# Optimization experiments

Measured on AMD Instinct MI355X. Metric: run time of the kernel, lower is better.

Reference implementation:

```python
import jax, jax.numpy as jnp
import numpy as np

D_MODEL = 1024
NHEAD = 16
HEAD_DIM = D_MODEL // NHEAD
D_FF = 4096
EPS = 1e-8


def rmsnorm(x, w):
    # matches torch: norm = ||x||_2 / sqrt(d); out = w * x / (rms + eps)
    rms = jnp.linalg.norm(x, axis=-1, keepdims=True) / np.sqrt(x.shape[-1])
    return w * (x / (rms + EPS))


def setup_inputs() -> dict:
    key = jax.random.key(0)
    ks = jax.random.split(key, 11)
    B, S = 4, 2048
    init = lambda k, shape, fan_in: jax.random.uniform(k, shape, jnp.float32, -1.0, 1.0) / np.sqrt(fan_in)
    return {
        "src": jax.random.normal(ks[0], (B, S, D_MODEL), jnp.float32),
        "qkv_w": init(ks[1], (D_MODEL, 3 * D_MODEL), D_MODEL),
        "qkv_b": init(ks[2], (3 * D_MODEL,), D_MODEL),
        "out_w": init(ks[3], (D_MODEL, D_MODEL), D_MODEL),
        "out_b": init(ks[4], (D_MODEL,), D_MODEL),
        "ff1_w": init(ks[5], (D_MODEL, D_FF), D_MODEL),
        "ff1_b": init(ks[6], (D_FF,), D_MODEL),
        "ff2_w": init(ks[7], (D_FF, D_MODEL), D_FF),
        "ff2_b": init(ks[8], (D_MODEL,), D_FF),
        "norm1_w": jnp.ones((D_MODEL,), jnp.float32),
        "norm2_w": jnp.ones((D_MODEL,), jnp.float32),
    }


def reference(src, qkv_w, qkv_b, out_w, out_b, ff1_w, ff1_b, ff2_w, ff2_b, norm1_w, norm2_w):
    B, S, _ = src.shape
    # --- pre-norm attention block ---
    x = rmsnorm(src, norm1_w)
    qkv = x @ qkv_w + qkv_b                     # [B,S,3*D]
    qkv = qkv.reshape(B, S, 3, NHEAD, HEAD_DIM)
    q, k, v = qkv[:, :, 0], qkv[:, :, 1], qkv[:, :, 2]   # [B,S,H,D]
    scores = jnp.einsum('bshd,bthd->bhst', q, k) / np.sqrt(HEAD_DIM)
    attn = jax.nn.softmax(scores, axis=-1)
    ctx = jnp.einsum('bhst,bthd->bshd', attn, v).reshape(B, S, D_MODEL)
    src = src + ctx @ out_w + out_b
    # --- pre-norm FFN block ---
    y = rmsnorm(src, norm2_w)
    h = jax.nn.gelu(y @ ff1_w + ff1_b, approximate=False)
    src = src + h @ ff2_w + ff2_b
    return src
```

## Files before the change

### kernel.cpp

```cpp
#include <hip/hip_runtime.h>
#include <hip/hip_bf16.h>

#define DM   1024
#define DFF  4096
#define NH   16
#define HD   64
#define SEQ  2048
#define BATCH 4
#define NTOK (BATCH*SEQ)

typedef float  f32x4  __attribute__((ext_vector_type(4)));
typedef short  bf16x8 __attribute__((ext_vector_type(8)));

#define SBAR() asm volatile("s_barrier" ::: "memory")
#define S_VMCNT(N) asm volatile("s_waitcnt vmcnt(" #N ")" ::: "memory")

__device__ __forceinline__ unsigned short f2bf(float f) {
    unsigned int x = __builtin_bit_cast(unsigned int, f);
    x += 0x7fff + ((x >> 16) & 1);
    return (unsigned short)(x >> 16);
}

__device__ __forceinline__ float fexp2(float x) {
    float r; asm("v_exp_f32 %0, %1" : "=v"(r) : "v"(x)); return r;
}
__device__ __forceinline__ float fmax3(float a, float b, float c) {
    float r; asm("v_max3_f32 %0, %1, %2, %3" : "=v"(r) : "v"(a), "v"(b), "v"(c)); return r;
}

__device__ __forceinline__ void gload_lds16(const void* g, void* l) {
    __builtin_amdgcn_global_load_lds(
        (const __attribute__((address_space(1))) unsigned int*)g,
        (__attribute__((address_space(3))) unsigned int*)l,
        16, 0, 0);
}

__device__ __forceinline__ int swz(int row, int elem) { return elem ^ ((row & 7) << 3); }

__global__ __launch_bounds__(256)
void convT_kernel(const float* __restrict__ W, unsigned short* __restrict__ Wt, int K, int N)
{
    __shared__ float tile[32][33];
    int n0 = blockIdx.x * 32, k0 = blockIdx.y * 32;
    int tx = threadIdx.x & 31, ty = threadIdx.x >> 5;
    #pragma unroll
    for (int i = 0; i < 4; ++i)
        tile[ty + i*8][tx] = W[(size_t)(k0 + ty + i*8) * N + n0 + tx];
    __syncthreads();
    #pragma unroll
    for (int i = 0; i < 4; ++i)
        Wt[(size_t)(n0 + ty + i*8) * K + k0 + tx] = f2bf(tile[tx][ty + i*8]);
}

__global__ __launch_bounds__(256)
void rmsnorm_kernel(const float* __restrict__ in, const float* __restrict__ w,
                    unsigned short* __restrict__ out)
{
    __shared__ float red[4];
    int row = blockIdx.x, t = threadIdx.x;
    float4 v = ((const float4*)(in + (size_t)row * DM))[t];
    float ss = v.x*v.x + v.y*v.y + v.z*v.z + v.w*v.w;
    #pragma unroll
    for (int m = 1; m < 64; m <<= 1) ss += __shfl_xor(ss, m);
    if ((t & 63) == 0) red[t >> 6] = ss;
    __syncthreads();
    float tot = red[0] + red[1] + red[2] + red[3];
    float rms = sqrtf(tot) * (1.f / 32.f);
    float inv = 1.f / (rms + 1e-8f);
    float4 wv = ((const float4*)w)[t];
    unsigned int lo = (unsigned int)f2bf(v.x*inv*wv.x) | ((unsigned int)f2bf(v.y*inv*wv.y) << 16);
    unsigned int hi = (unsigned int)f2bf(v.z*inv*wv.z) | ((unsigned int)f2bf(v.w*inv*wv.w) << 16);
    uint2 pk; pk.x = lo; pk.y = hi;
    *(uint2*)(out + (size_t)row * DM + t * 4) = pk;
}

template<int MODE, int NB>
__global__ __launch_bounds__(512, 2)
void gemm_tpl(const unsigned short* __restrict__ A,
              const unsigned short* __restrict__ Bt,
              const float* __restrict__ bias,
              int N, int K, int nx,
              const float* __restrict__ resid,
              float* __restrict__ outf,
              unsigned short* __restrict__ outb,
              unsigned short* __restrict__ q,
              unsigned short* __restrict__ kk,
              unsigned short* __restrict__ vt)
{
    constexpr int NJ = NB / 64;
    constexpr int WN = NB / 4;
    __shared__ __align__(16) unsigned short Atile[2][2][256 * 32];
    __shared__ __align__(16) unsigned short Btile[2][2][NB * 32];
    const int tid = threadIdx.x, w = tid >> 6, l = tid & 63;
    const int lr = l & 15, lh = l >> 4;
    const int wm = w >> 2, wn = w & 3;
    const int nwg = gridDim.x, cpx = nwg >> 3;
    const int sid = (blockIdx.x & 7) * cpx + (blockIdx.x >> 3);
    const int by = sid / nx, bx = sid - by * nx;
    const int m0 = by * 256, n0 = bx * NB;
    const int nkt = K >> 6;
    const int srow = w * 16 + (l >> 2);
    const int scol = (((l & 3) ^ (srow & 3)) << 3);

    auto stageA = [&](int kt, int ks, int half, int bi) {
        int r0 = half * 128;
        gload_lds16(A + (size_t)(m0 + r0 + srow) * K + kt * 64 + ks * 32 + scol,
                    &Atile[bi][ks][(r0 + w * 16) * 32]);
    };
    auto stageB = [&](int kt, int ks, int half, int bi) {
        int r0 = half * 128;
        gload_lds16(Bt + (size_t)(n0 + r0 + srow) * K + kt * 64 + ks * 32 + scol,
                    &Btile[bi][ks][(r0 + w * 16) * 32]);
    };

    f32x4 acc[8][NJ];
    #pragma unroll
    for (int a = 0; a < 8; ++a)
        #pragma unroll
        for (int j = 0; j < NJ; ++j) acc[a][j] = {0.f, 0.f, 0.f, 0.f};

    #pragma unroll
    for (int ks = 0; ks < 2; ++ks) {
        stageA(0, ks, 0, 0); stageA(0, ks, 1, 0);
        stageB(0, ks, 0, 0);
        if (NB == 256) stageB(0, ks, 1, 0);
    }

    int bi = 0;
    for (int t = 0; t < nkt; ++t) {
        #pragma unroll
        for (int ks = 0; ks < 2; ++ks) {
            if (ks == 0 || t + 1 < nkt) {
                if constexpr (NB == 256) { S_VMCNT(4); } else { S_VMCNT(3); }
            } else {
                S_VMCNT(0);
            }
            SBAR();
            bf16x8 bB[NJ];
            #pragma unroll
            for (int j = 0; j < NJ; ++j) {
                int row = wn * WN + j * 16 + lr;
                bB[j] = *(const bf16x8*)&Btile[bi][ks][row * 32 + ((lh ^ (row & 3)) << 3)];
            }
            #pragma unroll
            for (int rho = 0; rho < 2; ++rho) {
                bf16x8 aA[4];
                #pragma unroll
                for (int i = 0; i < 4; ++i) {
                    int row = wm * 128 + rho * 64 + i * 16 + lr;
                    aA[i] = *(const bf16x8*)&Atile[bi][ks][row * 32 + ((lh ^ (row & 3)) << 3)];
                }
                if (t + 1 < nkt) {
                    if (rho == 0) { stageA(t + 1, ks, 0, bi ^ 1); stageA(t + 1, ks, 1, bi ^ 1); }
                    else          { stageB(t + 1, ks, 0, bi ^ 1);
                                    if (NB == 256) stageB(t + 1, ks, 1, bi ^ 1); }
                }
                SBAR();
                __builtin_amdgcn_s_setprio(1);
                #pragma unroll
                for (int i = 0; i < 4; ++i)
                    #pragma unroll
                    for (int j = 0; j < NJ; ++j)
                        acc[rho * 4 + i][j] = __builtin_amdgcn_mfma_f32_16x16x32_bf16(
                            aA[i], bB[j], acc[rho * 4 + i][j], 0, 0, 0);
                __builtin_amdgcn_s_setprio(0);
            }
        }
        bi ^= 1;
    }

    #pragma unroll
    for (int a = 0; a < 8; ++a) {
        const int rho = a >> 2, i = a & 3;
        #pragma unroll
        for (int j = 0; j < NJ; ++j) {
            #pragma unroll
            for (int r = 0; r < 4; ++r) {
                int row = m0 + wm * 128 + rho * 64 + i * 16 + lh * 4 + r;
                int col = n0 + wn * WN + j * 16 + lr;
                float v = acc[a][j][r] + bias[col];
                if (MODE == 0) {
                    int wh = col >> 10, h = (col >> 6) & 15, d = col & 63;
                    int b = row >> 11, s = row & 2047;
                    size_t base = (size_t)(b * NH + h);
                    if (wh == 0)      q [(base * SEQ + s) * HD + d] = f2bf(v * 0.18033688f);
                    else if (wh == 1) kk[(base * SEQ + s) * HD + d] = f2bf(v);
                    else              vt[(base * HD + d) * SEQ + s] = f2bf(v);
                } else if (MODE == 2) {
                    float g = 0.5f * v * (1.f + erff(v * 0.70710678118f));
                    outb[(size_t)row * N + col] = f2bf(g);
                } else {
                    outf[(size_t)row * N + col] = v + resid[(size_t)row * N + col];
                }
            }
        }
    }
}

__global__ __launch_bounds__(256, 3)
void attn_kernel(const unsigned short* __restrict__ q,
                 const unsigned short* __restrict__ k,
                 const unsigned short* __restrict__ vt,
                 unsigned short* __restrict__ ctx)
{
    __shared__ __align__(16) unsigned short Ks[2][64 * 64];
    __shared__ __align__(16) unsigned short Vs[2][64 * 64];
    __shared__ __align__(16) unsigned short PQ[4][32 * 64];

    const int tid = threadIdx.x, w = tid >> 6, l = tid & 63;
    const int lr = l & 15, lh = l >> 4;

    const int sid = (blockIdx.x & 7) * 128 + (blockIdx.x >> 3);
    const int bh = sid >> 4, qt = sid & 15;
    const int b = bh >> 4, h = bh & 15;

    const int rloc = l >> 3;
    const int cswz = (((l & 7) ^ rloc) << 3);

    const unsigned short* kbase0 = k  + (size_t)bh * SEQ * HD;
    const unsigned short* vbase0 = vt + (size_t)bh * HD * SEQ;
    const int NT = SEQ / 64;

    auto stageK = [&](int t, int buf) {
        const unsigned short* kb = kbase0 + (size_t)t * 64 * HD;
        #pragma unroll
        for (int c = 0; c < 2; ++c) {
            int r0 = (w * 2 + c) * 8;
            gload_lds16(kb + (size_t)(r0 + rloc) * HD + cswz, &Ks[buf][r0 * 64]);
        }
    };
    auto stageV = [&](int t, int buf) {
        const unsigned short* vb = vbase0 + t * 64;
        #pragma unroll
        for (int c = 0; c < 2; ++c) {
            int d0 = w * 16 + c * 8;
            gload_lds16(vb + (size_t)(d0 + rloc) * SEQ + cswz, &Vs[buf][d0 * 64]);
        }
    };

    unsigned short* Pw = &PQ[w][0];
    const unsigned short* qbase = q + ((size_t)bh * SEQ + qt * 128 + w * 32) * HD;
    #pragma unroll
    for (int c = 0; c < 4; ++c) {
        int r0 = c * 8;
        gload_lds16(qbase + (size_t)(r0 + rloc) * HD + cswz, &Pw[r0 * 64]);
    }
    stageK(0, 0);
    stageV(0, 0);
    S_VMCNT(4);
    bf16x8 aq[2][2];
    #pragma unroll
    for (int g = 0; g < 2; ++g) {
        int row = g * 16 + lr;
        aq[g][0] = *(const bf16x8*)&Pw[row * 64 + swz(row,      lh * 8)];
        aq[g][1] = *(const bf16x8*)&Pw[row * 64 + swz(row, 32 + lh * 8)];
    }
    __syncthreads();

    float mrow[2] = {-1e30f, -1e30f}, lrow[2] = {0.f, 0.f};
    f32x4 o[2][4];
    #pragma unroll
    for (int g = 0; g < 2; ++g)
        #pragma unroll
        for (int nf = 0; nf < 4; ++nf) o[g][nf] = {0.f, 0.f, 0.f, 0.f};

    for (int t = 0; t < NT; ++t) {
        const int cur = t & 1;
        if (t + 1 < NT) { stageK(t + 1, cur ^ 1); stageV(t + 1, cur ^ 1); }

        const unsigned short* Kc = &Ks[cur][0];
        const unsigned short* Vc = &Vs[cur][0];

        f32x4 sc[2][4];
        __builtin_amdgcn_s_setprio(1);
        #pragma unroll
        for (int j = 0; j < 4; ++j) {
            int kr = j * 16 + lr;
            bf16x8 kb0 = *(const bf16x8*)&Kc[kr * 64 + swz(kr,      lh * 8)];
            bf16x8 kb1 = *(const bf16x8*)&Kc[kr * 64 + swz(kr, 32 + lh * 8)];
            #pragma unroll
            for (int g = 0; g < 2; ++g) {
                f32x4 z = {0.f, 0.f, 0.f, 0.f};
                z = __builtin_amdgcn_mfma_f32_16x16x32_bf16(kb0, aq[g][0], z, 0, 0, 0);
                z = __builtin_amdgcn_mfma_f32_16x16x32_bf16(kb1, aq[g][1], z, 0, 0, 0);
                sc[g][j] = z;
            }
        }
        __builtin_amdgcn_s_setprio(0);

        #pragma unroll
        for (int g = 0; g < 2; ++g) {
            float mt = fmax3(sc[g][0][0], sc[g][0][1], sc[g][0][2]);
            mt = fmax3(mt, sc[g][0][3], sc[g][1][0]);
            mt = fmax3(mt, sc[g][1][1], sc[g][1][2]);
            mt = fmax3(mt, sc[g][1][3], sc[g][2][0]);
            mt = fmax3(mt, sc[g][2][1], sc[g][2][2]);
            mt = fmax3(mt, sc[g][2][3], sc[g][3][0]);
            mt = fmax3(mt, sc[g][3][1], sc[g][3][2]);
            mt = fmaxf(mt, sc[g][3][3]);
            mt = fmaxf(mt, __shfl_xor(mt, 16));
            mt = fmaxf(mt, __shfl_xor(mt, 32));

            float al = 1.f;
            if (!__all(mt <= mrow[g] + 8.f)) {
                float mnew = fmaxf(mrow[g], mt);
                al = fexp2(mrow[g] - mnew);
                mrow[g] = mnew;
                float alo[4];
                #pragma unroll
                for (int r = 0; r < 4; ++r) alo[r] = __shfl(al, lh * 4 + r);
                #pragma unroll
                for (int nf = 0; nf < 4; ++nf)
                    #pragma unroll
                    for (int r = 0; r < 4; ++r) o[g][nf][r] *= alo[r];
            }

            float rs = 0.f;
            int prow = g * 16 + lr;
            #pragma unroll
            for (int j = 0; j < 4; ++j) {
                float p0 = fexp2(sc[g][j][0] - mrow[g]), p1 = fexp2(sc[g][j][1] - mrow[g]);
                float p2 = fexp2(sc[g][j][2] - mrow[g]), p3 = fexp2(sc[g][j][3] - mrow[g]);
                rs += (p0 + p1) + (p2 + p3);
                unsigned int w0, w1;
                asm("v_cvt_pk_bf16_f32 %0, %1, %2" : "=v"(w0) : "v"(p0), "v"(p1));
                asm("v_cvt_pk_bf16_f32 %0, %1, %2" : "=v"(w1) : "v"(p2), "v"(p3));
                int k0 = j * 16 + lh * 4;
                int e = prow * 64 + (k0 ^ ((prow & 7) << 3));
                *(unsigned int*)&Pw[e]     = w0;
                *(unsigned int*)&Pw[e + 2] = w1;
            }
            rs += __shfl_xor(rs, 16);
            rs += __shfl_xor(rs, 32);
            lrow[g] = lrow[g] * al + rs;
        }

        bf16x8 ap[2][2];
        #pragma unroll
        for (int g = 0; g < 2; ++g) {
            int prow = g * 16 + lr;
            ap[g][0] = *(const bf16x8*)&Pw[prow * 64 + swz(prow,      lh * 8)];
            ap[g][1] = *(const bf16x8*)&Pw[prow * 64 + swz(prow, 32 + lh * 8)];
        }

        __builtin_amdgcn_s_setprio(1);
        #pragma unroll
        for (int nf = 0; nf < 4; ++nf) {
            int vr = nf * 16 + lr;
            bf16x8 vb0 = *(const bf16x8*)&Vc[vr * 64 + swz(vr,      lh * 8)];
            bf16x8 vb1 = *(const bf16x8*)&Vc[vr * 64 + swz(vr, 32 + lh * 8)];
            #pragma unroll
            for (int g = 0; g < 2; ++g) {
                o[g][nf] = __builtin_amdgcn_mfma_f32_16x16x32_bf16(ap[g][0], vb0, o[g][nf], 0, 0, 0);
                o[g][nf] = __builtin_amdgcn_mfma_f32_16x16x32_bf16(ap[g][1], vb1, o[g][nf], 0, 0, 0);
            }
        }
        __builtin_amdgcn_s_setprio(0);

        __syncthreads();
    }

    #pragma unroll
    for (int g = 0; g < 2; ++g) {
        float linv = 1.f / lrow[g];
        float lo4[4];
        #pragma unroll
        for (int r = 0; r < 4; ++r) lo4[r] = __shfl(linv, lh * 4 + r);
        #pragma unroll
        for (int nf = 0; nf < 4; ++nf)
            #pragma unroll
            for (int r = 0; r < 4; ++r) {
                int row = qt * 128 + w * 32 + g * 16 + lh * 4 + r;
                ctx[((size_t)b * SEQ + row) * DM + h * 64 + nf * 16 + lr] =
                    f2bf(o[g][nf][r] * lo4[r]);
            }
    }
}

extern "C" void kernel_launch(void* const* d_in, const int* in_sizes, int n_in,
                              void* d_out, int out_size, void* d_ws, size_t ws_size,
                              hipStream_t stream)
{
    const float* src   = (const float*)d_in[0];
    const float* qkv_w = (const float*)d_in[1];
    const float* qkv_b = (const float*)d_in[2];
    const float* out_w = (const float*)d_in[3];
    const float* out_b = (const float*)d_in[4];
    const float* ff1_w = (const float*)d_in[5];
    const float* ff1_b = (const float*)d_in[6];
    const float* ff2_w = (const float*)d_in[7];
    const float* ff2_b = (const float*)d_in[8];
    const float* n1_w  = (const float*)d_in[9];
    const float* n2_w  = (const float*)d_in[10];

    char* ws = (char*)d_ws;
    const size_t MB = 1u << 20;
    unsigned short* qkv_wt = (unsigned short*)(ws);
    unsigned short* out_wt = (unsigned short*)(ws + 6*MB);
    unsigned short* ff1_wt = (unsigned short*)(ws + 8*MB);
    unsigned short* ff2_wt = (unsigned short*)(ws + 16*MB);
    unsigned short* xb     = (unsigned short*)(ws + 24*MB);
    unsigned short* qb     = (unsigned short*)(ws + 40*MB);
    unsigned short* kb     = (unsigned short*)(ws + 56*MB);
    unsigned short* vtb    = (unsigned short*)(ws + 72*MB);
    unsigned short* hb     = (unsigned short*)(ws + 24*MB);
    unsigned short* ctxb   = (unsigned short*)(ws + 88*MB);
    unsigned short* yb     = (unsigned short*)(ws + 88*MB);
    float*          src2   = (float*)(ws + 104*MB);
    float* outp = (float*)d_out;

    convT_kernel<<<dim3(3072/32, 1024/32), 256, 0, stream>>>(qkv_w, qkv_wt, 1024, 3072);
    convT_kernel<<<dim3(1024/32, 1024/32), 256, 0, stream>>>(out_w, out_wt, 1024, 1024);
    convT_kernel<<<dim3(4096/32, 1024/32), 256, 0, stream>>>(ff1_w, ff1_wt, 1024, 4096);
    convT_kernel<<<dim3(1024/32, 4096/32), 256, 0, stream>>>(ff2_w, ff2_wt, 4096, 1024);

    rmsnorm_kernel<<<NTOK, 256, 0, stream>>>(src, n1_w, xb);

    gemm_tpl<0, 128><<<768, 512, 0, stream>>>(xb, qkv_wt, qkv_b, 3072, 1024, 24,
                                              nullptr, nullptr, nullptr, qb, kb, vtb);

    attn_kernel<<<SEQ/128 * BATCH*NH, 256, 0, stream>>>(qb, kb, vtb, ctxb);

    gemm_tpl<3, 128><<<256, 512, 0, stream>>>(ctxb, out_wt, out_b, 1024, 1024, 8,
                                              src, src2, nullptr, nullptr, nullptr, nullptr);

    rmsnorm_kernel<<<NTOK, 256, 0, stream>>>(src2, n2_w, yb);

    gemm_tpl<2, 256><<<512, 512, 0, stream>>>(yb, ff1_wt, ff1_b, 4096, 1024, 16,
                                              nullptr, nullptr, hb, nullptr, nullptr, nullptr);

    gemm_tpl<3, 128><<<256, 512, 0, stream>>>(hb, ff2_wt, ff2_b, 1024, 4096, 8,
                                              src2, outp, nullptr, nullptr, nullptr, nullptr);
}
```

Baseline: 463.9 us.

## Triple-buffer GEMM tiles and fix N-tile at 128 for all GEMMs

The GEMM moves from double to triple buffering of LDS tiles. Loads for k-step t+2 are issued while computing t, and the vmcnt waits are adjusted so more global-to-LDS traffic is in flight, hiding memory latency. The template drops the NB=256 variant, so FF1 now runs with 128-wide N tiles on 1024 blocks. LDS use grows to about 144KB per block, which with launch_bounds(512,2) may limit occupancy to one block per CU. The smaller FF1 tile also lowers data reuse.

```diff
diff --git a/kernel.cpp b/kernel.cpp
--- a/kernel.cpp
+++ b/kernel.cpp
@@ -74,7 +74,7 @@
     *(uint2*)(out + (size_t)row * DM + t * 4) = pk;
 }
 
-template<int MODE, int NB>
+template<int MODE>
 __global__ __launch_bounds__(512, 2)
 void gemm_tpl(const unsigned short* __restrict__ A,
               const unsigned short* __restrict__ Bt,
@@ -87,17 +87,17 @@
               unsigned short* __restrict__ kk,
               unsigned short* __restrict__ vt)
 {
-    constexpr int NJ = NB / 64;
-    constexpr int WN = NB / 4;
-    __shared__ __align__(16) unsigned short Atile[2][2][256 * 32];
-    __shared__ __align__(16) unsigned short Btile[2][2][NB * 32];
+    constexpr int NJ = 2;
+    constexpr int WN = 32;
+    __shared__ __align__(16) unsigned short Atile[3][2][256 * 32];
+    __shared__ __align__(16) unsigned short Btile[3][2][128 * 32];
     const int tid = threadIdx.x, w = tid >> 6, l = tid & 63;
     const int lr = l & 15, lh = l >> 4;
     const int wm = w >> 2, wn = w & 3;
     const int nwg = gridDim.x, cpx = nwg >> 3;
     const int sid = (blockIdx.x & 7) * cpx + (blockIdx.x >> 3);
     const int by = sid / nx, bx = sid - by * nx;
-    const int m0 = by * 256, n0 = bx * NB;
+    const int m0 = by * 256, n0 = bx * 128;
     const int nkt = K >> 6;
     const int srow = w * 16 + (l >> 2);
     const int scol = (((l & 3) ^ (srow & 3)) << 3);
@@ -107,10 +107,9 @@
         gload_lds16(A + (size_t)(m0 + r0 + srow) * K + kt * 64 + ks * 32 + scol,
                     &Atile[bi][ks][(r0 + w * 16) * 32]);
     };
-    auto stageB = [&](int kt, int ks, int half, int bi) {
-        int r0 = half * 128;
-        gload_lds16(Bt + (size_t)(n0 + r0 + srow) * K + kt * 64 + ks * 32 + scol,
-                    &Btile[bi][ks][(r0 + w * 16) * 32]);
+    auto stageB = [&](int kt, int ks, int bi) {
+        gload_lds16(Bt + (size_t)(n0 + srow) * K + kt * 64 + ks * 32 + scol,
+                    &Btile[bi][ks][(w * 16) * 32]);
     };
 
     f32x4 acc[8][NJ];
@@ -120,20 +119,21 @@
         for (int j = 0; j < NJ; ++j) acc[a][j] = {0.f, 0.f, 0.f, 0.f};
 
     #pragma unroll
-    for (int ks = 0; ks < 2; ++ks) {
-        stageA(0, ks, 0, 0); stageA(0, ks, 1, 0);
-        stageB(0, ks, 0, 0);
-        if (NB == 256) stageB(0, ks, 1, 0);
-    }
+    for (int ks = 0; ks < 2; ++ks) { stageA(0, ks, 0, 0); stageA(0, ks, 1, 0); stageB(0, ks, 0); }
+    #pragma unroll
+    for (int ks = 0; ks < 2; ++ks) { stageA(1, ks, 0, 1); stageA(1, ks, 1, 1); stageB(1, ks, 1); }
 
     int bi = 0;
     for (int t = 0; t < nkt; ++t) {
+        const int wbuf = (bi + 2 >= 3) ? bi - 1 : bi + 2;
         #pragma unroll
         for (int ks = 0; ks < 2; ++ks) {
-            if (ks == 0 || t + 1 < nkt) {
-                if constexpr (NB == 256) { S_VMCNT(4); } else { S_VMCNT(3); }
+            if (ks == 0) {
+                if (t + 1 < nkt) { S_VMCNT(9); } else { S_VMCNT(3); }
             } else {
-                S_VMCNT(0);
+                if (t + 2 < nkt)      { S_VMCNT(9); }
+                else if (t + 1 < nkt) { S_VMCNT(6); }
+                else                  { S_VMCNT(0); }
             }
             SBAR();
             bf16x8 bB[NJ];
@@ -150,10 +150,9 @@
                     int row = wm * 128 + rho * 64 + i * 16 + lr;
                     aA[i] = *(const bf16x8*)&Atile[bi][ks][row * 32 + ((lh ^ (row & 3)) << 3)];
                 }
-                if (t + 1 < nkt) {
-                    if (rho == 0) { stageA(t + 1, ks, 0, bi ^ 1); stageA(t + 1, ks, 1, bi ^ 1); }
-                    else          { stageB(t + 1, ks, 0, bi ^ 1);
-                                    if (NB == 256) stageB(t + 1, ks, 1, bi ^ 1); }
+                if (t + 2 < nkt) {
+                    if (rho == 0) { stageA(t + 2, ks, 0, wbuf); stageA(t + 2, ks, 1, wbuf); }
+                    else          { stageB(t + 2, ks, wbuf); }
                 }
                 SBAR();
                 __builtin_amdgcn_s_setprio(1);
@@ -166,7 +165,7 @@
                 __builtin_amdgcn_s_setprio(0);
             }
         }
-        bi ^= 1;
+        bi = (bi + 1 == 3) ? 0 : bi + 1;
     }
 
     #pragma unroll
@@ -416,19 +415,19 @@
 
     rmsnorm_kernel<<<NTOK, 256, 0, stream>>>(src, n1_w, xb);
 
-    gemm_tpl<0, 128><<<768, 512, 0, stream>>>(xb, qkv_wt, qkv_b, 3072, 1024, 24,
-                                              nullptr, nullptr, nullptr, qb, kb, vtb);
+    gemm_tpl<0><<<768, 512, 0, stream>>>(xb, qkv_wt, qkv_b, 3072, 1024, 24,
+                                         nullptr, nullptr, nullptr, qb, kb, vtb);
 
     attn_kernel<<<SEQ/128 * BATCH*NH, 256, 0, stream>>>(qb, kb, vtb, ctxb);
 
-    gemm_tpl<3, 128><<<256, 512, 0, stream>>>(ctxb, out_wt, out_b, 1024, 1024, 8,
-                                              src, src2, nullptr, nullptr, nullptr, nullptr);
+    gemm_tpl<3><<<256, 512, 0, stream>>>(ctxb, out_wt, out_b, 1024, 1024, 8,
+                                         src, src2, nullptr, nullptr, nullptr, nullptr);
 
     rmsnorm_kernel<<<NTOK, 256, 0, stream>>>(src2, n2_w, yb);
 
-    gemm_tpl<2, 256><<<512, 512, 0, stream>>>(yb, ff1_wt, ff1_b, 4096, 1024, 16,
-                                              nullptr, nullptr, hb, nullptr, nullptr, nullptr);
-
-    gemm_tpl<3, 128><<<256, 512, 0, stream>>>(hb, ff2_wt, ff2_b, 1024, 4096, 8,
-                                              src2, outp, nullptr, nullptr, nullptr, nullptr);
-}
+    gemm_tpl<2><<<1024, 512, 0, stream>>>(yb, ff1_wt, ff1_b, 4096, 1024, 32,
+                                          nullptr, nullptr, hb, nullptr, nullptr, nullptr);
+
+    gemm_tpl<3><<<256, 512, 0, stream>>>(hb, ff2_wt, ff2_b, 1024, 4096, 8,
+                                         src2, outp, nullptr, nullptr, nullptr, nullptr);
+}
```

New measurement: 494.4 us. 1.07x slower.
